# Kernel optimization log

Measured on AMD Instinct MI355X. Metric: run time of the kernel, lower is better.

Reference implementation:

```python
import jax, jax.numpy as jnp
import numpy as np

N = 100000
E = 1600000
NFEAT, NHID1, NHID2, NCLASS, NSTRUC = 512, 256, 128, 40, 128


def glorot(key, shape):
    lim = 1.0 / np.sqrt(shape[0])
    return jax.random.uniform(key, shape, jnp.float32, -lim, lim)


def setup_inputs() -> dict:
    key = jax.random.key(0)
    ks = jax.random.split(key, 12)
    x = jax.random.normal(ks[0], (N, NFEAT), jnp.float32)
    edge_index = jax.random.randint(ks[1], (2, E), 0, N, jnp.int32)
    edge_weight = jax.random.uniform(ks[2], (E,), jnp.float32)
    return {
        "x": x,
        "edge_index": edge_index,
        "edge_weight": edge_weight,
        "W1": glorot(ks[3], (NFEAT, NHID1)), "b1": jnp.zeros((NHID1,), jnp.float32),
        "W2": glorot(ks[4], (NHID1, NHID2)), "b2": jnp.zeros((NHID2,), jnp.float32),
        "W3": glorot(ks[5], (NHID2, NCLASS)), "b3": jnp.zeros((NCLASS,), jnp.float32),
        "We": glorot(ks[6], (NHID1, NSTRUC)), "be": jnp.zeros((NSTRUC,), jnp.float32),
    }


def spmm(edge_index, edge_weight, support):
    # adj @ support with adj given as weighted edge list (dst <- src)
    src, dst = edge_index[0], edge_index[1]
    msgs = support[src] * edge_weight[:, None]  # [E, d]
    return jax.ops.segment_sum(msgs, dst, num_segments=N)


def gc_layer(x, edge_index, edge_weight, W, b):
    support = x @ W
    return spmm(edge_index, edge_weight, support) + b


def reference(x, edge_index, edge_weight, W1, b1, W2, b2, W3, b3, We, be):
    # eval mode: dropout is identity
    h = jax.nn.relu(gc_layer(x, edge_index, edge_weight, W1, b1))
    out1 = jax.nn.relu(gc_layer(h, edge_index, edge_weight, W2, b2))
    out1 = gc_layer(out1, edge_index, edge_weight, W3, b3)
    out2 = h @ We + be
    return jax.nn.log_softmax(out1, axis=1), out2
```

## Files before the change

### kernel.cpp

```cpp
#include <hip/hip_runtime.h>
#include <hip/hip_bf16.h>

#define NNODES 100000
#define NEDGES 1600000
#define BSH 7
#define NBUCK ((NNODES + 127) >> 7)
#define SPBLK 1536

typedef __attribute__((ext_vector_type(8))) short bf16x8;
typedef __attribute__((ext_vector_type(4))) short bf16x4;
typedef __attribute__((ext_vector_type(2))) short bf16x2;
typedef __attribute__((ext_vector_type(4))) float f32x4;
typedef __attribute__((ext_vector_type(2))) float f32x2;

static __device__ __forceinline__ short f2bf(float f) {
  __hip_bfloat16 b = __float2bfloat16(f);
  return __builtin_bit_cast(short, b);
}
static __device__ __forceinline__ float bf2f(short s) {
  unsigned int u = ((unsigned int)(unsigned short)s) << 16;
  return __builtin_bit_cast(float, u);
}
static __device__ __forceinline__ void fma4(f32x4& a, float w, bf16x4 v) {
  a[0] = fmaf(w, bf2f(v[0]), a[0]);
  a[1] = fmaf(w, bf2f(v[1]), a[1]);
  a[2] = fmaf(w, bf2f(v[2]), a[2]);
  a[3] = fmaf(w, bf2f(v[3]), a[3]);
}
static __device__ __forceinline__ void fma2(f32x2& a, float w, bf16x2 v) {
  a[0] = fmaf(w, bf2f(v[0]), a[0]);
  a[1] = fmaf(w, bf2f(v[1]), a[1]);
}

__global__ void wtrans_kernel(const float* __restrict__ W, short* __restrict__ Wt,
                              int K, int Nvalid, int Npad) {
  int idx = blockIdx.x * blockDim.x + threadIdx.x;
  if (idx >= Npad * K) return;
  int n = idx / K, k = idx - n * K;
  Wt[idx] = (n < Nvalid) ? f2bf(W[(size_t)k * Nvalid + n]) : (short)0;
}

__global__ void bcount_kernel(const int* __restrict__ ei, int* __restrict__ bcnt) {
  __shared__ int h[NBUCK];
  for (int i = threadIdx.x; i < NBUCK; i += 256) h[i] = 0;
  __syncthreads();
  int stride = gridDim.x * 256;
  for (int e = blockIdx.x * 256 + threadIdx.x; e < NEDGES; e += stride)
    atomicAdd(&h[ei[NEDGES + e] >> BSH], 1);
  __syncthreads();
  for (int i = threadIdx.x; i < NBUCK; i += 256)
    if (h[i]) atomicAdd(&bcnt[i], h[i]);
}

__global__ void bscan_kernel(const int* __restrict__ bcnt, int* __restrict__ bbase,
                             int* __restrict__ bcur, int* __restrict__ rowptr) {
  __shared__ int lds[1024];
  int t = threadIdx.x;
  int c = (t < NBUCK) ? bcnt[t] : 0;
  lds[t] = c;
  __syncthreads();
  for (int off = 1; off < 1024; off <<= 1) {
    int v = (t >= off) ? lds[t - off] : 0;
    __syncthreads();
    lds[t] += v;
    __syncthreads();
  }
  if (t < NBUCK) {
    int ex = lds[t] - c;
    bbase[t] = ex;
    bcur[t] = ex;
  }
  if (t == NBUCK) bbase[t] = NEDGES;
  if (t == 0) rowptr[NNODES] = NEDGES;
}

#define P4CHUNK 8192
__global__ void bscatter_kernel(const int* __restrict__ ei, const float* __restrict__ ew,
                                int* __restrict__ bcur, int2* __restrict__ tmp) {
  __shared__ int cnt[NBUCK];
  __shared__ int pos[NBUCK];
  int tid = threadIdx.x;
  for (int i = tid; i < NBUCK; i += 256) cnt[i] = 0;
  __syncthreads();
  int base = blockIdx.x * P4CHUNK;
  int end = base + P4CHUNK;
  if (end > NEDGES) end = NEDGES;
  for (int e = base + tid; e < end; e += 256)
    atomicAdd(&cnt[ei[NEDGES + e] >> BSH], 1);
  __syncthreads();
  for (int i = tid; i < NBUCK; i += 256)
    if (cnt[i]) pos[i] = atomicAdd(&bcur[i], cnt[i]);
  __syncthreads();
  for (int e = base + tid; e < end; e += 256) {
    int d = ei[NEDGES + e];
    int b = d >> BSH;
    int p = atomicAdd(&pos[b], 1);
    tmp[p] = make_int2(ei[e] | ((d & 127) << 17), __float_as_int(ew[e]));
  }
}

__global__ void bsort_kernel(const int* __restrict__ bbase, const int2* __restrict__ tmp,
                             int2* __restrict__ edat, int* __restrict__ rowptr) {
  __shared__ int hist[128];
  __shared__ int cur[128];
  int b = blockIdx.x;
  int tid = threadIdx.x;
  int base = bbase[b], cnt = bbase[b + 1] - base;
  if (tid < 128) hist[tid] = 0;
  __syncthreads();
  for (int i = tid; i < cnt; i += 256)
    atomicAdd(&hist[(tmp[base + i].x >> 17) & 127], 1);
  __syncthreads();
  int c = (tid < 128) ? hist[tid] : 0;
  if (tid < 128) cur[tid] = c;
  __syncthreads();
  for (int off = 1; off < 128; off <<= 1) {
    int v = (tid < 128 && tid >= off) ? cur[tid - off] : 0;
    __syncthreads();
    if (tid < 128) cur[tid] += v;
    __syncthreads();
  }
  if (tid < 128) {
    int ex = cur[tid] - c;
    int node = (b << BSH) + tid;
    if (node < NNODES) rowptr[node] = base + ex;
    cur[tid] = base + ex;
  }
  __syncthreads();
  for (int i = tid; i < cnt; i += 256) {
    int2 r = tmp[base + i];
    int d = (r.x >> 17) & 127;
    int p = atomicAdd(&cur[d], 1);
    edat[p] = make_int2(r.x & 0x1FFFF, r.y);
  }
}

#define LDSTR 72
template <bool AF32, int EPI>
__launch_bounds__(256, 2)
__global__ void gemm_tiled(const void* __restrict__ Aptr, int K,
                           const short* __restrict__ Wt,
                           void* __restrict__ Cp0, float* __restrict__ Cp1,
                           const float* __restrict__ bias, int nvalid, int ldc) {
  __shared__ __align__(16) short As[128 * LDSTR];
  __shared__ __align__(16) short Bs[128 * LDSTR];
  int tid = threadIdx.x;
  int lane = tid & 63, wv = tid >> 6;
  int wr = wv >> 1, wc = wv & 1;
  int m0 = blockIdx.y * 128;
  int n0 = blockIdx.x * 128;
  f32x4 acc[4][4];
#pragma unroll
  for (int i = 0; i < 4; i++)
#pragma unroll
    for (int j = 0; j < 4; j++) acc[i][j] = (f32x4){0.f, 0.f, 0.f, 0.f};

  int srow = tid >> 3;
  int scol = (tid & 7) * 8;

  for (int k0 = 0; k0 < K; k0 += 64) {
#pragma unroll
    for (int p = 0; p < 4; p++) {
      int ml = p * 32 + srow;
      int arow = m0 + ml;
      if (arow >= NNODES) arow = NNODES - 1;
      bf16x8 av;
      if (AF32) {
        const float* ap = (const float*)Aptr + (size_t)arow * K + k0 + scol;
        f32x4 a0 = *(const f32x4*)ap;
        f32x4 a1 = *(const f32x4*)(ap + 4);
#pragma unroll
        for (int j = 0; j < 4; j++) { av[j] = f2bf(a0[j]); av[4 + j] = f2bf(a1[j]); }
      } else {
        av = *(const bf16x8*)((const short*)Aptr + (size_t)arow * K + k0 + scol);
      }
      *(bf16x8*)&As[ml * LDSTR + scol] = av;
      bf16x8 bv = *(const bf16x8*)(Wt + (size_t)(n0 + ml) * K + k0 + scol);
      *(bf16x8*)&Bs[ml * LDSTR + scol] = bv;
    }
    __syncthreads();
    int r = lane & 15, quad = lane >> 4;
#pragma unroll
    for (int kk = 0; kk < 64; kk += 32) {
      bf16x8 af[4], bfr[4];
#pragma unroll
      for (int i = 0; i < 4; i++)
        af[i] = *(const bf16x8*)&As[(wr * 64 + i * 16 + r) * LDSTR + kk + quad * 8];
#pragma unroll
      for (int j = 0; j < 4; j++)
        bfr[j] = *(const bf16x8*)&Bs[(wc * 64 + j * 16 + r) * LDSTR + kk + quad * 8];
#pragma unroll
      for (int i = 0; i < 4; i++)
#pragma unroll
        for (int j = 0; j < 4; j++)
          acc[i][j] = __builtin_amdgcn_mfma_f32_16x16x32_bf16(af[i], bfr[j], acc[i][j], 0, 0, 0);
    }
    __syncthreads();
  }

  int quad = lane >> 4, cl = lane & 15;
#pragma unroll
  for (int i = 0; i < 4; i++) {
    int rowb = m0 + wr * 64 + i * 16 + quad * 4;
#pragma unroll
    for (int rr = 0; rr < 4; rr++) {
      int row = rowb + rr;
      if (row < NNODES) {
#pragma unroll
        for (int j = 0; j < 4; j++) {
          int col = n0 + wc * 64 + j * 16 + cl;
          float v = acc[i][j][rr];
          if (EPI == 0) {
            ((short*)Cp0)[(size_t)row * ldc + col] = f2bf(v);
          } else if (EPI == 1) {
            if (col < nvalid) Cp1[(size_t)row * nvalid + col] = v;
          } else {
            if (col < 128) ((short*)Cp0)[(size_t)row * 128 + col] = f2bf(v);
            else Cp1[(size_t)row * 128 + (col - 128)] = v + bias[col - 128];
          }
        }
      }
    }
  }
}


template <int NE>
static __device__ __forceinline__ void gat1(int2 me, int b, const short* Sc,
                                            f32x4& acc0, f32x4& acc1) {
  int src[NE]; float wt[NE]; bf16x4 v[NE];
#pragma unroll
  for (int j = 0; j < NE; j++) {
    src[j] = __builtin_amdgcn_readlane(me.x, b + j);
    wt[j] = __builtin_bit_cast(float, __builtin_amdgcn_readlane(me.y, b + j));
  }
#pragma unroll
  for (int j = 0; j < NE; j++) v[j] = *(const bf16x4*)(Sc + (size_t)src[j] * 256);
#pragma unroll
  for (int j = 0; j < NE; j++) {
    if (j & 1) fma4(acc1, wt[j], v[j]); else fma4(acc0, wt[j], v[j]);
  }
}

template <int NE>
static __device__ __forceinline__ void gat2(int2 me, int b, const short* Sc,
                                            f32x2& acc0, f32x2& acc1) {
  int src[NE]; float wt[NE]; bf16x2 v[NE];
#pragma unroll
  for (int j = 0; j < NE; j++) {
    src[j] = __builtin_amdgcn_readlane(me.x, b + j);
    wt[j] = __builtin_bit_cast(float, __builtin_amdgcn_readlane(me.y, b + j));
  }
#pragma unroll
  for (int j = 0; j < NE; j++) v[j] = *(const bf16x2*)(Sc + (size_t)src[j] * 128);
#pragma unroll
  for (int j = 0; j < NE; j++) {
    if (j & 1) fma2(acc1, wt[j], v[j]); else fma2(acc0, wt[j], v[j]);
  }
}

template <int NE>
static __device__ __forceinline__ void gat3(int2 me, int b, const float* S3l,
                                            float& acc0, float& acc1) {
  int src[NE]; float wt[NE]; float v[NE];
#pragma unroll
  for (int j = 0; j < NE; j++) {
    src[j] = __builtin_amdgcn_readlane(me.x, b + j);
    wt[j] = __builtin_bit_cast(float, __builtin_amdgcn_readlane(me.y, b + j));
  }
#pragma unroll
  for (int j = 0; j < NE; j++) v[j] = S3l[(size_t)src[j] * 40];
#pragma unroll
  for (int j = 0; j < NE; j++) {
    if (j & 1) acc1 = fmaf(wt[j], v[j], acc1); else acc0 = fmaf(wt[j], v[j], acc0);
  }
}

__launch_bounds__(256, 6)
__global__ void spmm1_kernel(const int* __restrict__ rowptr, const int2* __restrict__ edat,
                             const short* __restrict__ S,
                             const float* __restrict__ bias, short* __restrict__ H) {
  int nw = gridDim.x * 4;
  int wid = blockIdx.x * 4 + (threadIdx.x >> 6);
  int lane = threadIdx.x & 63;
  int c0 = lane * 4;
  const short* Sc = S + c0;
  f32x4 bv = *(const f32x4*)(bias + c0);
  for (int node = wid; node < NNODES; node += nw) {
    f32x4 acc0 = (f32x4){0.f, 0.f, 0.f, 0.f};
    f32x4 acc1 = (f32x4){0.f, 0.f, 0.f, 0.f};
    int beg = rowptr[node], end = rowptr[node + 1];
    for (int w0 = beg; w0 < end; w0 += 64) {
      int wcnt = end - w0;
      if (wcnt > 64) wcnt = 64;
      int2 me = (lane < wcnt) ? edat[w0 + lane] : make_int2(0, 0);
      int g16 = wcnt >> 4, rem = wcnt & 15;
      int b = 0;
      for (int g = 0; g < g16; ++g, b += 16) gat1<16>(me, b, Sc, acc0, acc1);
      if (rem) {
        if (rem > 8) gat1<16>(me, b, Sc, acc0, acc1);
        else gat1<8>(me, b, Sc, acc0, acc1);
      }
    }
    bf16x4 h;
#pragma unroll
    for (int j = 0; j < 4; j++) h[j] = f2bf(fmaxf(acc0[j] + acc1[j] + bv[j], 0.f));
    *(bf16x4*)(H + (size_t)node * 256 + c0) = h;
  }
}

__launch_bounds__(256, 6)
__global__ void spmm2_kernel(const int* __restrict__ rowptr, const int2* __restrict__ edat,
                             const short* __restrict__ S,
                             const float* __restrict__ bias, short* __restrict__ H) {
  int nw = gridDim.x * 4;
  int wid = blockIdx.x * 4 + (threadIdx.x >> 6);
  int lane = threadIdx.x & 63;
  int c0 = lane * 2;
  const short* Sc = S + c0;
  float b0 = bias[c0], b1 = bias[c0 + 1];
  for (int node = wid; node < NNODES; node += nw) {
    f32x2 acc0 = (f32x2){0.f, 0.f};
    f32x2 acc1 = (f32x2){0.f, 0.f};
    int beg = rowptr[node], end = rowptr[node + 1];
    for (int w0 = beg; w0 < end; w0 += 64) {
      int wcnt = end - w0;
      if (wcnt > 64) wcnt = 64;
      int2 me = (lane < wcnt) ? edat[w0 + lane] : make_int2(0, 0);
      int g16 = wcnt >> 4, rem = wcnt & 15;
      int b = 0;
      for (int g = 0; g < g16; ++g, b += 16) gat2<16>(me, b, Sc, acc0, acc1);
      if (rem) {
        if (rem > 8) gat2<16>(me, b, Sc, acc0, acc1);
        else gat2<8>(me, b, Sc, acc0, acc1);
      }
    }
    bf16x2 h;
    h[0] = f2bf(fmaxf(acc0[0] + acc1[0] + b0, 0.f));
    h[1] = f2bf(fmaxf(acc0[1] + acc1[1] + b1, 0.f));
    *(bf16x2*)(H + (size_t)node * 128 + c0) = h;
  }
}

__launch_bounds__(256, 6)
__global__ void spmm3_kernel(const int* __restrict__ rowptr, const int2* __restrict__ edat,
                             const float* __restrict__ S3,
                             const float* __restrict__ b3, float* __restrict__ out1) {
  int nw = gridDim.x * 4;
  int wid = blockIdx.x * 4 + (threadIdx.x >> 6);
  int lane = threadIdx.x & 63;
  bool act = lane < 40;
  const float* S3l = S3 + lane;
  float bl = act ? b3[lane] : 0.f;
  for (int node = wid; node < NNODES; node += nw) {
    float acc0 = 0.f, acc1 = 0.f;
    int beg = rowptr[node], end = rowptr[node + 1];
    for (int w0 = beg; w0 < end; w0 += 64) {
      int wcnt = end - w0;
      if (wcnt > 64) wcnt = 64;
      int2 me = (lane < wcnt) ? edat[w0 + lane] : make_int2(0, 0);
      int g16 = wcnt >> 4, rem = wcnt & 15;
      int b = 0;
      for (int g = 0; g < g16; ++g, b += 16) gat3<16>(me, b, S3l, acc0, acc1);
      if (rem) {
        if (rem > 8) gat3<16>(me, b, S3l, acc0, acc1);
        else gat3<8>(me, b, S3l, acc0, acc1);
      }
    }
    float acc = acc0 + acc1 + bl;
    float v = act ? acc : -__builtin_inff();
    for (int off = 32; off > 0; off >>= 1) v = fmaxf(v, __shfl_xor(v, off));
    float e = act ? expf(acc - v) : 0.f;
    for (int off = 32; off > 0; off >>= 1) e += __shfl_xor(e, off);
    float ls = logf(e);
    if (act) out1[(size_t)node * 40 + lane] = acc - v - ls;
  }
}

extern "C" void kernel_launch(void* const* d_in, const int* in_sizes, int n_in,
                              void* d_out, int out_size, void* d_ws, size_t ws_size,
                              hipStream_t stream) {
  const float* x  = (const float*)d_in[0];
  const int*   ei = (const int*)d_in[1];
  const float* ew = (const float*)d_in[2];
  const float* W1 = (const float*)d_in[3];
  const float* b1 = (const float*)d_in[4];
  const float* W2 = (const float*)d_in[5];
  const float* b2 = (const float*)d_in[6];
  const float* W3 = (const float*)d_in[7];
  const float* b3 = (const float*)d_in[8];
  const float* We = (const float*)d_in[9];
  const float* be = (const float*)d_in[10];
  float* out1 = (float*)d_out;
  float* out2 = (float*)d_out + (size_t)NNODES * 40;

  char* w = (char*)d_ws;
  size_t off = 0;
  auto alloc = [&](size_t bytes) -> char* {
    char* p = w + off;
    off += (bytes + 255) & ~(size_t)255;
    return p;
  };
  int*   rowptr = (int*)alloc((size_t)(NNODES + 1) * 4);
  int*   bcnt   = (int*)alloc((size_t)NBUCK * 4);
  int*   bbase  = (int*)alloc((size_t)(NBUCK + 1) * 4);
  int*   bcur   = (int*)alloc((size_t)NBUCK * 4);
  int2*  edat   = (int2*)alloc((size_t)NEDGES * 8);
  short* Wt1    = (short*)alloc((size_t)256 * 512 * 2);
  short* Wt2e   = (short*)alloc((size_t)256 * 256 * 2);
  short* Wt3    = (short*)alloc((size_t)128 * 128 * 2);
  short* S1bf   = (short*)alloc((size_t)NNODES * 256 * 2);
  short* Hbf    = (short*)alloc((size_t)NNODES * 256 * 2);
  short* S2bf   = (short*)alloc((size_t)NNODES * 128 * 2);
  short* Tbf    = (short*)alloc((size_t)NNODES * 128 * 2);
  float* S3     = (float*)alloc(((size_t)NNODES * 40 + 64) * 4);
  int2*  tmp    = (int2*)S3;

  hipMemsetAsync(bcnt, 0, (size_t)NBUCK * 4, stream);
  bcount_kernel<<<256, 256, 0, stream>>>(ei, bcnt);
  bscan_kernel<<<1, 1024, 0, stream>>>(bcnt, bbase, bcur, rowptr);
  bscatter_kernel<<<(NEDGES + P4CHUNK - 1) / P4CHUNK, 256, 0, stream>>>(ei, ew, bcur, tmp);
  bsort_kernel<<<NBUCK, 256, 0, stream>>>(bbase, tmp, edat, rowptr);

  wtrans_kernel<<<(256 * 512 + 255) / 256, 256, 0, stream>>>(W1, Wt1, 512, 256, 256);
  wtrans_kernel<<<(128 * 256 + 255) / 256, 256, 0, stream>>>(W2, Wt2e, 256, 128, 128);
  wtrans_kernel<<<(128 * 256 + 255) / 256, 256, 0, stream>>>(We, Wt2e + (size_t)128 * 256, 256, 128, 128);
  wtrans_kernel<<<(128 * 128 + 255) / 256, 256, 0, stream>>>(W3, Wt3, 128, 40, 128);

  int gblocks = (NNODES + 127) / 128;

  gemm_tiled<true, 0><<<dim3(2, gblocks), 256, 0, stream>>>(x, 512, Wt1, S1bf, nullptr, nullptr, 256, 256);
  spmm1_kernel<<<SPBLK, 256, 0, stream>>>(rowptr, edat, S1bf, b1, Hbf);
  gemm_tiled<false, 2><<<dim3(2, gblocks), 256, 0, stream>>>(Hbf, 256, Wt2e, S2bf, out2, be, 256, 128);
  spmm2_kernel<<<SPBLK, 256, 0, stream>>>(rowptr, edat, S2bf, b2, Tbf);
  gemm_tiled<false, 1><<<dim3(1, gblocks), 256, 0, stream>>>(Tbf, 128, Wt3, nullptr, S3, nullptr, 40, 40);
  spmm3_kernel<<<SPBLK, 256, 0, stream>>>(rowptr, edat, S3, b3, out1);
}
```

Measured before the change: 757.7 us.

## Load bf16 GEMM tiles directly to LDS with XOR-swizzled layout

For the bf16-input GEMM path and the weight tiles, the per-thread global-load-then-LDS-store staging is replaced by global_load_lds direct transfers into unpadded 64-wide LDS tiles. To avoid bank conflicts without padding, an XOR swizzle on 8-element chunks is applied both at the producers (the weight transpose kernel and the SpMM output writes of H) and at the MFMA fragment reads. This removes VGPR round-trips and LDS padding, but couples the stored layout of H and Wt to the GEMM's read pattern, so any other consumer of those buffers must use the same swizzle.

New measurement: 734.1 us. 3.1% less time.

```diff
diff --git a/kernel.cpp b/kernel.cpp
--- a/kernel.cpp
+++ b/kernel.cpp
@@ -32,12 +32,19 @@
   a[1] = fmaf(w, bf2f(v[1]), a[1]);
 }
 
+static __device__ __forceinline__ void gload16(const void* g, void* l) {
+  __builtin_amdgcn_global_load_lds(
+      (const __attribute__((address_space(1))) unsigned int*)g,
+      (__attribute__((address_space(3))) unsigned int*)l, 16, 0, 0);
+}
+
 __global__ void wtrans_kernel(const float* __restrict__ W, short* __restrict__ Wt,
                               int K, int Nvalid, int Npad) {
   int idx = blockIdx.x * blockDim.x + threadIdx.x;
   if (idx >= Npad * K) return;
   int n = idx / K, k = idx - n * K;
-  Wt[idx] = (n < Nvalid) ? f2bf(W[(size_t)k * Nvalid + n]) : (short)0;
+  int ks = (k & ~63) | ((((k >> 3) & 7) ^ (n & 7)) << 3) | (k & 7);
+  Wt[idx] = (n < Nvalid) ? f2bf(W[(size_t)ks * Nvalid + n]) : (short)0;
 }
 
 __global__ void bcount_kernel(const int* __restrict__ ei, int* __restrict__ bcnt) {
@@ -142,8 +149,8 @@
                            const short* __restrict__ Wt,
                            void* __restrict__ Cp0, float* __restrict__ Cp1,
                            const float* __restrict__ bias, int nvalid, int ldc) {
-  __shared__ __align__(16) short As[128 * LDSTR];
-  __shared__ __align__(16) short Bs[128 * LDSTR];
+  __shared__ __align__(16) short As[128 * (AF32 ? LDSTR : 64)];
+  __shared__ __align__(16) short Bs[128 * 64];
   int tid = threadIdx.x;
   int lane = tid & 63, wv = tid >> 6;
   int wr = wv >> 1, wc = wv & 1;
@@ -159,36 +166,52 @@
   int scol = (tid & 7) * 8;
 
   for (int k0 = 0; k0 < K; k0 += 64) {
-#pragma unroll
-    for (int p = 0; p < 4; p++) {
-      int ml = p * 32 + srow;
-      int arow = m0 + ml;
-      if (arow >= NNODES) arow = NNODES - 1;
-      bf16x8 av;
-      if (AF32) {
+    if constexpr (AF32) {
+#pragma unroll
+      for (int p = 0; p < 4; p++) {
+        int ml = p * 32 + srow;
+        int arow = m0 + ml;
+        if (arow >= NNODES) arow = NNODES - 1;
         const float* ap = (const float*)Aptr + (size_t)arow * K + k0 + scol;
         f32x4 a0 = *(const f32x4*)ap;
         f32x4 a1 = *(const f32x4*)(ap + 4);
+        bf16x8 av;
 #pragma unroll
         for (int j = 0; j < 4; j++) { av[j] = f2bf(a0[j]); av[4 + j] = f2bf(a1[j]); }
-      } else {
-        av = *(const bf16x8*)((const short*)Aptr + (size_t)arow * K + k0 + scol);
-      }
-      *(bf16x8*)&As[ml * LDSTR + scol] = av;
-      bf16x8 bv = *(const bf16x8*)(Wt + (size_t)(n0 + ml) * K + k0 + scol);
-      *(bf16x8*)&Bs[ml * LDSTR + scol] = bv;
+        *(bf16x8*)&As[ml * LDSTR + scol] = av;
+      }
+    } else {
+#pragma unroll
+      for (int p = 0; p < 4; p++) {
+        int row = p * 32 + wv * 8 + (lane >> 3);
+        int arow = m0 + row;
+        if (arow >= NNODES) arow = NNODES - 1;
+        gload16((const short*)Aptr + (size_t)arow * K + k0 + (lane & 7) * 8,
+                &As[p * 2048 + wv * 512]);
+      }
+    }
+#pragma unroll
+    for (int p = 0; p < 4; p++) {
+      int row = p * 32 + wv * 8 + (lane >> 3);
+      gload16(Wt + (size_t)(n0 + row) * K + k0 + (lane & 7) * 8,
+              &Bs[p * 2048 + wv * 512]);
     }
     __syncthreads();
     int r = lane & 15, quad = lane >> 4;
 #pragma unroll
     for (int kk = 0; kk < 64; kk += 32) {
+      int csw = (kk + quad * 8) ^ ((r & 7) << 3);
       bf16x8 af[4], bfr[4];
 #pragma unroll
-      for (int i = 0; i < 4; i++)
-        af[i] = *(const bf16x8*)&As[(wr * 64 + i * 16 + r) * LDSTR + kk + quad * 8];
+      for (int i = 0; i < 4; i++) {
+        if constexpr (AF32)
+          af[i] = *(const bf16x8*)&As[(wr * 64 + i * 16 + r) * LDSTR + kk + quad * 8];
+        else
+          af[i] = *(const bf16x8*)&As[((wr * 64 + i * 16 + r) << 6) + csw];
+      }
 #pragma unroll
       for (int j = 0; j < 4; j++)
-        bfr[j] = *(const bf16x8*)&Bs[(wc * 64 + j * 16 + r) * LDSTR + kk + quad * 8];
+        bfr[j] = *(const bf16x8*)&Bs[((wc * 64 + j * 16 + r) << 6) + csw];
 #pragma unroll
       for (int i = 0; i < 4; i++)
 #pragma unroll
@@ -305,7 +328,8 @@
     bf16x4 h;
 #pragma unroll
     for (int j = 0; j < 4; j++) h[j] = f2bf(fmaxf(acc0[j] + acc1[j] + bv[j], 0.f));
-    *(bf16x4*)(H + (size_t)node * 256 + c0) = h;
+    int c0w = ((lane >> 4) << 6) + ((((lane >> 1) & 7) ^ (node & 7)) << 3) + ((lane & 1) << 2);
+    *(bf16x4*)(H + (size_t)node * 256 + c0w) = h;
   }
 }
 
@@ -338,7 +362,8 @@
     bf16x2 h;
     h[0] = f2bf(fmaxf(acc0[0] + acc1[0] + b0, 0.f));
     h[1] = f2bf(fmaxf(acc0[1] + acc1[1] + b1, 0.f));
-    *(bf16x2*)(H + (size_t)node * 128 + c0) = h;
+    int c0w = ((lane >> 5) << 6) + ((((lane >> 2) & 7) ^ (node & 7)) << 3) + ((lane & 3) << 1);
+    *(bf16x2*)(H + (size_t)node * 128 + c0w) = h;
   }
 }
 
```
